# Optimization experiments

Hardware: AMD Instinct MI355X
Metric: run time of the kernel (lower is better)

The kernel has to match this reference:

```python
import jax, jax.numpy as jnp
import numpy as np

N = 50000          # num nodes
E = 800000         # num edges (before self loops)
IN_C = 128
HID = 256          # heads * head_dim
HEADS = 4
HEAD_DIM = HID // HEADS
OUT_C = 64
NEG_SLOPE = 0.2    # PyG GATConv default leaky_relu slope
BN_EPS = 1e-5


def _gat_conv(x, src, dst, W, att_src, att_dst, bias, concat):
    """PyG-style GATConv (with self loops already appended to src/dst).
    x: [N, in_c]; W: [in_c, H*C]; att_src/att_dst: [H, C]; bias: [H*C] or [C]."""
    H, C = att_src.shape
    h = (x @ W).reshape(-1, H, C)                               # [N, H, C]
    a_src = jnp.einsum('nhc,hc->nh', h, att_src)                # [N, H]
    a_dst = jnp.einsum('nhc,hc->nh', h, att_dst)                # [N, H]
    e = jax.nn.leaky_relu(a_src[src] + a_dst[dst], NEG_SLOPE)   # [Et, H]
    # segment softmax over destination nodes (numerically stable)
    m = jax.ops.segment_max(e, dst, num_segments=N)             # [N, H]
    m = jnp.where(jnp.isfinite(m), m, 0.0)
    ex = jnp.exp(e - m[dst])
    denom = jax.ops.segment_sum(ex, dst, num_segments=N)        # [N, H]
    alpha = ex / (denom[dst] + 1e-16)                           # [Et, H]
    msg = alpha[:, :, None] * h[src]                            # [Et, H, C]
    out = jax.ops.segment_sum(msg, dst, num_segments=N)         # [N, H, C]
    out = out.reshape(N, H * C) if concat else out.mean(axis=1)
    return out + bias


def _bn_eval(x, gamma, beta, mean, var):
    return (x - mean) * jax.lax.rsqrt(var + BN_EPS) * gamma + beta


def setup_inputs() -> dict:
    key = jax.random.key(0)
    ks = jax.random.split(key, 16)
    x = jax.random.normal(ks[0], (N, IN_C), dtype=jnp.float32)
    edge_index = jax.random.randint(ks[1], (2, E), 0, N, dtype=jnp.int64)

    def lin(k, fan_in, fan_out):
        s = (1.0 / np.sqrt(fan_in)).astype(np.float32)
        return jax.random.normal(k, (fan_in, fan_out), dtype=jnp.float32) * s

    def att(k, h, c):
        return jax.random.normal(k, (h, c), dtype=jnp.float32) * 0.1

    return {
        'x': x, 'edge_index': edge_index,
        'W0': lin(ks[2], IN_C, HID), 'as0': att(ks[3], HEADS, HEAD_DIM), 'ad0': att(ks[4], HEADS, HEAD_DIM), 'b0': jnp.zeros((HID,), jnp.float32),
        'bn0_g': jnp.ones((HID,), jnp.float32), 'bn0_b': jnp.zeros((HID,), jnp.float32), 'bn0_m': jnp.zeros((HID,), jnp.float32), 'bn0_v': jnp.ones((HID,), jnp.float32),
        'W1': lin(ks[5], HID, HID), 'as1': att(ks[6], HEADS, HEAD_DIM), 'ad1': att(ks[7], HEADS, HEAD_DIM), 'b1': jnp.zeros((HID,), jnp.float32),
        'bn1_g': jnp.ones((HID,), jnp.float32), 'bn1_b': jnp.zeros((HID,), jnp.float32), 'bn1_m': jnp.zeros((HID,), jnp.float32), 'bn1_v': jnp.ones((HID,), jnp.float32),
        'W2': lin(ks[8], HID, OUT_C), 'as2': att(ks[9], 1, OUT_C), 'ad2': att(ks[10], 1, OUT_C), 'b2': jnp.zeros((OUT_C,), jnp.float32),
    }


def reference(x, edge_index, W0, as0, ad0, b0, bn0_g, bn0_b, bn0_m, bn0_v,
              W1, as1, ad1, b1, bn1_g, bn1_b, bn1_m, bn1_v,
              W2, as2, ad2, b2):
    loop = jnp.arange(N, dtype=edge_index.dtype)
    src = jnp.concatenate([edge_index[0], loop])   # PyG add_self_loops=True
    dst = jnp.concatenate([edge_index[1], loop])

    h = _gat_conv(x, src, dst, W0, as0, ad0, b0, concat=True)
    h = jax.nn.elu(_bn_eval(h, bn0_g, bn0_b, bn0_m, bn0_v))   # dropout: eval -> identity
    h = _gat_conv(h, src, dst, W1, as1, ad1, b1, concat=True)
    h = jax.nn.elu(_bn_eval(h, bn1_g, bn1_b, bn1_m, bn1_v))
    out = _gat_conv(h, src, dst, W2, as2, ad2, b2, concat=False)  # heads=1, mean
    return out
```

## Files before the change

### kernel.cpp

```cpp
#include <hip/hip_runtime.h>

#define NN   50000
#define EE   800000
#define ET   850000
#define INC  128
#define HID  256
#define OUTC 64
#define NEG  0.2f
#define BNEPS 1e-5f

typedef __bf16 bf16x8 __attribute__((ext_vector_type(8)));
typedef float  f32x4  __attribute__((ext_vector_type(4)));

static __device__ __forceinline__ float b2f(unsigned short u) {
    return __uint_as_float(((unsigned)u) << 16);
}
static __device__ __forceinline__ unsigned short f2b(float f) {
    unsigned u = __float_as_uint(f);
    unsigned r = u + 0x7FFFu + ((u >> 16) & 1u);
    return (unsigned short)(r >> 16);
}
static __device__ __forceinline__ float leaky(float x) {
    return x > 0.f ? x : NEG * x;
}
static __device__ __forceinline__ float ew(float e) {
    return __expf(fminf(e, 80.f));
}

__global__ void k_init(const int* __restrict__ ei, const unsigned* __restrict__ xw,
                       int* __restrict__ cnt, int* __restrict__ flagW, int* __restrict__ flagB,
                       int nbZ) {
    __shared__ int cs[4];
    int b = blockIdx.x, t = threadIdx.x;
    if (b < nbZ) {
        int i = b * 256 + t;
        if (i < NN) cnt[i] = 0;
    } else if (b == nbZ) {
        int c = 0;
        for (int k = 0; k < 16; k++) {
            int i = t + 256 * k;
            if (ei[2 * i + 1] != 0) c = 1;
        }
        for (int o = 1; o < 64; o <<= 1) c |= __shfl_xor(c, o);
        if ((t & 63) == 0) cs[t >> 6] = c;
        __syncthreads();
        if (t == 0) *flagW = cs[0] | cs[1] | cs[2] | cs[3];
    } else {
        int c = 0;
        for (int i = t; i < 4096; i += 256) {
            unsigned v = (xw[i] >> 8) & 0x7F;
            if (v >= 50 && v <= 67) c++;
        }
        for (int o = 1; o < 64; o <<= 1) c += __shfl_xor(c, o);
        if ((t & 63) == 0) cs[t >> 6] = c;
        __syncthreads();
        if (t == 0) *flagB = (cs[0] + cs[1] + cs[2] + cs[3] > 2048) ? 1 : 0;
    }
}

__global__ void k_params(const void* p0, const void* p1, const void* p2, const void* p3,
                         const void* p4, const void* p5, const void* p6, const void* p7,
                         const void* p8, const void* p9, const void* p10, const void* p11,
                         const void* p12, const void* p13, const void* p14, const void* p15,
                         const void* p16,
                         float* __restrict__ pp, const int* __restrict__ flagB) {
    const void* srcs[17] = {p0,p1,p2,p3,p4,p5,p6,p7,p8,p9,p10,p11,p12,p13,p14,p15,p16};
    int b = blockIdx.x, t = threadIdx.x;
    bool bf = (*flagB != 0);
    if (b < 14) {
        const void* s = srcs[b];
        pp[b * 256 + t] = bf ? b2f(((const unsigned short*)s)[t]) : ((const float*)s)[t];
    } else if (t < 192) {
        int arr = t >> 6, j = t & 63;
        const void* s = srcs[14 + arr];
        pp[14 * 256 + arr * 64 + j] = bf ? b2f(((const unsigned short*)s)[j]) : ((const float*)s)[j];
    }
}

__global__ void k_bulk(const void* __restrict__ W0, const void* __restrict__ W1,
                       const void* __restrict__ W2,
                       unsigned short* __restrict__ WT0, unsigned short* __restrict__ WT1,
                       unsigned short* __restrict__ WT2,
                       const void* __restrict__ x, unsigned short* __restrict__ xb,
                       const int* __restrict__ flagB) {
    int b = blockIdx.x, t = threadIdx.x;
    bool bf = (*flagB != 0);
    if (b < 128) {
        int i = b * 256 + t;
        int k = i >> 8, n = i & 255;
        unsigned short v = bf ? ((const unsigned short*)W0)[i] : f2b(((const float*)W0)[i]);
        WT0[n * INC + k] = v;
    } else if (b < 128 + 256) {
        int i = (b - 128) * 256 + t;
        int k = i >> 8, n = i & 255;
        unsigned short v = bf ? ((const unsigned short*)W1)[i] : f2b(((const float*)W1)[i]);
        WT1[n * HID + k] = v;
    } else if (b < 128 + 256 + 64) {
        int i = (b - 384) * 256 + t;
        int k = i >> 6, n = i & 63;
        unsigned short v = bf ? ((const unsigned short*)W2)[i] : f2b(((const float*)W2)[i]);
        WT2[n * HID + k] = v;
    } else {
        if (bf) return;
        int i = (b - 448) * 256 + t;
        if (i < NN * INC)
            xb[i] = f2b(((const float*)x)[i]);
    }
}

__global__ void k_hist(const int* __restrict__ ei, const int* __restrict__ flagW,
                       int* __restrict__ cnt) {
    int i = blockIdx.x * 256 + threadIdx.x;
    if (i >= ET) return;
    bool w32 = (*flagW != 0);
    int d = (i < EE) ? (w32 ? ei[EE + i] : ei[2 * (EE + i)]) : (i - EE);
    atomicAdd(&cnt[d], 1);
}

static __device__ __forceinline__ int block_scan_incl(int v, int t, int* ws) {
    int lane = t & 63, w = t >> 6;
    int x = v;
    for (int o = 1; o < 64; o <<= 1) {
        int y = __shfl_up(x, o);
        if (lane >= o) x += y;
    }
    if (lane == 63) ws[w] = x;
    __syncthreads();
    if (t == 0) {
        int s = 0;
        for (int k = 0; k < 4; k++) { int tmp = ws[k]; ws[k] = s; s += tmp; }
    }
    __syncthreads();
    return x + ws[w];
}

__global__ void k_scan_a(const int* __restrict__ cnt, int* __restrict__ rowptr, int* __restrict__ bsum) {
    __shared__ int ws[4];
    int t = threadIdx.x, b = blockIdx.x;
    int i = b * 256 + t;
    int v = (i < NN) ? cnt[i] : 0;
    int incl = block_scan_incl(v, t, ws);
    if (i < NN) rowptr[i] = incl - v;
    if (t == 255) bsum[b] = incl;
}

__global__ void k_scan_b(int* __restrict__ bsum, int nb) {
    __shared__ int ws[4];
    int t = threadIdx.x;
    int v = (t < nb) ? bsum[t] : 0;
    int incl = block_scan_incl(v, t, ws);
    if (t < nb) bsum[t] = incl - v;
}

__global__ void k_scan_c(int* __restrict__ rowptr, const int* __restrict__ bsum, int* __restrict__ cursor) {
    int t = threadIdx.x, b = blockIdx.x;
    int i = b * 256 + t;
    if (i < NN) {
        int r = rowptr[i] + bsum[b];
        rowptr[i] = r;
        cursor[i] = r;
    }
    if (i == 0) rowptr[NN] = ET;
}

__global__ void k_scatter(const int* __restrict__ ei, const int* __restrict__ flagW,
                          int* __restrict__ cursor, int* __restrict__ esrc) {
    int i = blockIdx.x * 256 + threadIdx.x;
    if (i >= ET) return;
    bool w32 = (*flagW != 0);
    int s, d;
    if (i < EE) {
        if (w32) { s = ei[i];     d = ei[EE + i]; }
        else     { s = ei[2 * i]; d = ei[2 * (EE + i)]; }
    } else {
        s = d = i - EE;
    }
    int p = atomicAdd(&cursor[d], 1);
    esrc[p] = s;
}

template<int NC, int NH>
__global__ __launch_bounds__(256) void k_gemm(const unsigned short* __restrict__ Amain,
                                              const void* __restrict__ Aalt,
                                              const int* __restrict__ flagB,
                                              const unsigned short* __restrict__ WT,
                                              unsigned short* __restrict__ H,
                                              float* __restrict__ asrc, float* __restrict__ adst,
                                              const float* __restrict__ asv, const float* __restrict__ adv,
                                              int M, int K) {
    __shared__ __align__(16) unsigned short As[128 * 40];
    __shared__ __align__(16) unsigned short Bs[64 * 40];
    const unsigned short* A = (*flagB) ? (const unsigned short*)Aalt : Amain;
    int t = threadIdx.x;
    int bm = blockIdx.x, bn = blockIdx.y;
    int lane = t & 63, wave = t >> 6;
    int m16 = lane & 15, quad = lane >> 4;

    f32x4 acc[2][4];
    for (int a = 0; a < 2; a++) for (int b = 0; b < 4; b++) acc[a][b] = (f32x4){0.f, 0.f, 0.f, 0.f};

    int arow = t >> 1, ahalf = t & 1;
    int brow = t >> 2, bq = t & 3;
    long gArow = (long)bm * 128 + arow;

    for (int k0 = 0; k0 < K; k0 += 32) {
        uint4 av0 = {0u, 0u, 0u, 0u}, av1 = {0u, 0u, 0u, 0u};
        if (gArow < M) {
            const unsigned short* ap = A + gArow * (size_t)K + k0 + ahalf * 16;
            av0 = *(const uint4*)(ap);
            av1 = *(const uint4*)(ap + 8);
        }
        uint4 bv = *(const uint4*)(WT + ((size_t)bn * 64 + brow) * K + k0 + bq * 8);
        *(uint4*)&As[arow * 40 + ahalf * 16]     = av0;
        *(uint4*)&As[arow * 40 + ahalf * 16 + 8] = av1;
        *(uint4*)&Bs[brow * 40 + bq * 8]         = bv;
        __syncthreads();
        int wrow = wave * 32;
        bf16x8 af[2], bf[4];
        for (int mt = 0; mt < 2; mt++)
            af[mt] = *(const bf16x8*)&As[(wrow + mt * 16 + m16) * 40 + quad * 8];
        for (int nt = 0; nt < 4; nt++)
            bf[nt] = *(const bf16x8*)&Bs[(nt * 16 + m16) * 40 + quad * 8];
        for (int mt = 0; mt < 2; mt++)
            for (int nt = 0; nt < 4; nt++)
                acc[mt][nt] = __builtin_amdgcn_mfma_f32_16x16x32_bf16(af[mt], bf[nt], acc[mt][nt], 0, 0, 0);
        __syncthreads();
    }

    float asc[4], adc[4];
    for (int nt = 0; nt < 4; nt++) {
        int col = bn * 64 + nt * 16 + m16;
        asc[nt] = asv[col];
        adc[nt] = adv[col];
    }
    for (int mt = 0; mt < 2; mt++) {
        int gR0 = bm * 128 + wave * 32 + mt * 16 + quad * 4;
        for (int r = 0; r < 4; r++) {
            int gR = gR0 + r;
            float ps = 0.f, pd = 0.f;
            for (int nt = 0; nt < 4; nt++) {
                float v = acc[mt][nt][r];
                ps += v * asc[nt];
                pd += v * adc[nt];
            }
            for (int o = 1; o < 16; o <<= 1) { ps += __shfl_xor(ps, o); pd += __shfl_xor(pd, o); }
            if (m16 == 0 && gR < M) {
                asrc[(size_t)gR * NH + bn] = ps;
                adst[(size_t)gR * NH + bn] = pd;
            }
            if (gR < M) {
                for (int nt = 0; nt < 4; nt++) {
                    int gC = bn * 64 + nt * 16 + m16;
                    H[(size_t)gR * NC + gC] = f2b(acc[mt][nt][r]);
                }
            }
        }
    }
}

__global__ void k_agg4(const unsigned short* __restrict__ h,
                       const float* __restrict__ asrc, const float* __restrict__ adst,
                       const int* __restrict__ rowptr, const int* __restrict__ esrc,
                       const float* __restrict__ bias,
                       const float* __restrict__ bng, const float* __restrict__ bnb,
                       const float* __restrict__ bnm, const float* __restrict__ bnv,
                       unsigned short* __restrict__ act) {
    int t = threadIdx.x;
    int wave = t >> 6, lane = t & 63;
    int node = blockIdx.x * 4 + wave;
    if (node >= NN) return;
    int e0 = rowptr[node], deg = rowptr[node + 1] - e0;
    int hd = lane >> 4, li = lane & 15;
    int wsel = lane & 48;
    float adh = adst[(size_t)node * 4 + hd];
    const size_t lc = (size_t)lane * 4;

    float den = 0.f, a0 = 0.f, a1 = 0.f, a2 = 0.f, a3 = 0.f;

    for (int c = 0; c < deg; c += 16) {
        int n = min(16, deg - c);
        float w = 0.f; int s = 0;
        if (li < n) {
            s = esrc[e0 + c + li];
            float e = asrc[(size_t)s * 4 + hd];
            w = ew(leaky(e + adh));
        }
        float wsum = w;
        wsum += __shfl_xor(wsum, 1);
        wsum += __shfl_xor(wsum, 2);
        wsum += __shfl_xor(wsum, 4);
        wsum += __shfl_xor(wsum, 8);
        den += wsum;
        int j = 0;
        for (; j + 8 <= n; j += 8) {
            int s0 = __shfl(s, j),     s1 = __shfl(s, j + 1);
            int s2 = __shfl(s, j + 2), s3 = __shfl(s, j + 3);
            int s4 = __shfl(s, j + 4), s5 = __shfl(s, j + 5);
            int s6 = __shfl(s, j + 6), s7 = __shfl(s, j + 7);
            float w0 = __shfl(w, wsel + j),     w1 = __shfl(w, wsel + j + 1);
            float w2 = __shfl(w, wsel + j + 2), w3 = __shfl(w, wsel + j + 3);
            float w4 = __shfl(w, wsel + j + 4), w5 = __shfl(w, wsel + j + 5);
            float w6 = __shfl(w, wsel + j + 6), w7 = __shfl(w, wsel + j + 7);
            ushort4 h0 = *(const ushort4*)(h + (size_t)s0 * HID + lc);
            ushort4 h1 = *(const ushort4*)(h + (size_t)s1 * HID + lc);
            ushort4 h2 = *(const ushort4*)(h + (size_t)s2 * HID + lc);
            ushort4 h3 = *(const ushort4*)(h + (size_t)s3 * HID + lc);
            ushort4 h4 = *(const ushort4*)(h + (size_t)s4 * HID + lc);
            ushort4 h5 = *(const ushort4*)(h + (size_t)s5 * HID + lc);
            ushort4 h6 = *(const ushort4*)(h + (size_t)s6 * HID + lc);
            ushort4 h7 = *(const ushort4*)(h + (size_t)s7 * HID + lc);
            a0 += w0 * b2f(h0.x) + w1 * b2f(h1.x) + w2 * b2f(h2.x) + w3 * b2f(h3.x)
                + w4 * b2f(h4.x) + w5 * b2f(h5.x) + w6 * b2f(h6.x) + w7 * b2f(h7.x);
            a1 += w0 * b2f(h0.y) + w1 * b2f(h1.y) + w2 * b2f(h2.y) + w3 * b2f(h3.y)
                + w4 * b2f(h4.y) + w5 * b2f(h5.y) + w6 * b2f(h6.y) + w7 * b2f(h7.y);
            a2 += w0 * b2f(h0.z) + w1 * b2f(h1.z) + w2 * b2f(h2.z) + w3 * b2f(h3.z)
                + w4 * b2f(h4.z) + w5 * b2f(h5.z) + w6 * b2f(h6.z) + w7 * b2f(h7.z);
            a3 += w0 * b2f(h0.w) + w1 * b2f(h1.w) + w2 * b2f(h2.w) + w3 * b2f(h3.w)
                + w4 * b2f(h4.w) + w5 * b2f(h5.w) + w6 * b2f(h6.w) + w7 * b2f(h7.w);
        }
        for (; j + 4 <= n; j += 4) {
            int s0 = __shfl(s, j),     s1 = __shfl(s, j + 1);
            int s2 = __shfl(s, j + 2), s3 = __shfl(s, j + 3);
            float w0 = __shfl(w, wsel + j),     w1 = __shfl(w, wsel + j + 1);
            float w2 = __shfl(w, wsel + j + 2), w3 = __shfl(w, wsel + j + 3);
            ushort4 h0 = *(const ushort4*)(h + (size_t)s0 * HID + lc);
            ushort4 h1 = *(const ushort4*)(h + (size_t)s1 * HID + lc);
            ushort4 h2 = *(const ushort4*)(h + (size_t)s2 * HID + lc);
            ushort4 h3 = *(const ushort4*)(h + (size_t)s3 * HID + lc);
            a0 += w0 * b2f(h0.x) + w1 * b2f(h1.x) + w2 * b2f(h2.x) + w3 * b2f(h3.x);
            a1 += w0 * b2f(h0.y) + w1 * b2f(h1.y) + w2 * b2f(h2.y) + w3 * b2f(h3.y);
            a2 += w0 * b2f(h0.z) + w1 * b2f(h1.z) + w2 * b2f(h2.z) + w3 * b2f(h3.z);
            a3 += w0 * b2f(h0.w) + w1 * b2f(h1.w) + w2 * b2f(h2.w) + w3 * b2f(h3.w);
        }
        for (; j < n; j++) {
            int sj = __shfl(s, j);
            float wj = __shfl(w, wsel + j);
            ushort4 hv = *(const ushort4*)(h + (size_t)sj * HID + lc);
            a0 += wj * b2f(hv.x); a1 += wj * b2f(hv.y);
            a2 += wj * b2f(hv.z); a3 += wj * b2f(hv.w);
        }
    }
    float inv = 1.f / (den + 1e-16f);
    int c0 = lane * 4;
    float o[4] = {a0 * inv, a1 * inv, a2 * inv, a3 * inv};
    unsigned short res[4];
    for (int j = 0; j < 4; j++) {
        int c = c0 + j;
        float val = o[j] + bias[c];
        val = (val - bnm[c]) * rsqrtf(bnv[c] + BNEPS) * bng[c] + bnb[c];
        val = val > 0.f ? val : expm1f(val);
        res[j] = f2b(val);
    }
    *(ushort4*)(act + (size_t)node * HID + c0) = *(ushort4*)res;
}

__global__ void k_agg1(const unsigned short* __restrict__ h,
                       const float* __restrict__ asrc, const float* __restrict__ adst,
                       const int* __restrict__ rowptr, const int* __restrict__ esrc,
                       const float* __restrict__ bias,
                       void* __restrict__ outp, const int* __restrict__ flagB) {
    int t = threadIdx.x;
    int wave = t >> 6, lane = t & 63;
    int node = blockIdx.x * 4 + wave;
    if (node >= NN) return;
    int e0 = rowptr[node], deg = rowptr[node + 1] - e0;
    float ad = adst[node];

    float den = 0.f, acc = 0.f;
    for (int c = 0; c < deg; c += 64) {
        int n = min(64, deg - c);
        float w = 0.f; int s = 0;
        if (lane < n) {
            s = esrc[e0 + c + lane];
            w = ew(leaky(asrc[s] + ad));
        }
        float wsum = w;
        for (int o = 1; o < 64; o <<= 1) wsum += __shfl_xor(wsum, o);
        den += wsum;
        int j = 0;
        for (; j + 8 <= n; j += 8) {
            int s0 = __shfl(s, j),     s1 = __shfl(s, j + 1);
            int s2 = __shfl(s, j + 2), s3 = __shfl(s, j + 3);
            int s4 = __shfl(s, j + 4), s5 = __shfl(s, j + 5);
            int s6 = __shfl(s, j + 6), s7 = __shfl(s, j + 7);
            float w0 = __shfl(w, j),     w1 = __shfl(w, j + 1);
            float w2 = __shfl(w, j + 2), w3 = __shfl(w, j + 3);
            float w4 = __shfl(w, j + 4), w5 = __shfl(w, j + 5);
            float w6 = __shfl(w, j + 6), w7 = __shfl(w, j + 7);
            float h0 = b2f(h[(size_t)s0 * OUTC + lane]);
            float h1 = b2f(h[(size_t)s1 * OUTC + lane]);
            float h2 = b2f(h[(size_t)s2 * OUTC + lane]);
            float h3 = b2f(h[(size_t)s3 * OUTC + lane]);
            float h4 = b2f(h[(size_t)s4 * OUTC + lane]);
            float h5 = b2f(h[(size_t)s5 * OUTC + lane]);
            float h6 = b2f(h[(size_t)s6 * OUTC + lane]);
            float h7 = b2f(h[(size_t)s7 * OUTC + lane]);
            acc += w0 * h0 + w1 * h1 + w2 * h2 + w3 * h3
                 + w4 * h4 + w5 * h5 + w6 * h6 + w7 * h7;
        }
        for (; j < n; j++) {
            int sj = __shfl(s, j);
            float wj = __shfl(w, j);
            acc += wj * b2f(h[(size_t)sj * OUTC + lane]);
        }
    }
    float val = acc / (den + 1e-16f) + bias[lane];
    if (*flagB) ((unsigned short*)outp)[(size_t)node * OUTC + lane] = f2b(val);
    else        ((float*)outp)[(size_t)node * OUTC + lane] = val;
}

extern "C" void kernel_launch(void* const* d_in, const int* in_sizes, int n_in,
                              void* d_out, int out_size, void* d_ws, size_t ws_size,
                              hipStream_t stream) {
    const void* x  = d_in[0];
    const int*  ei = (const int*)d_in[1];
    const void* W0 = d_in[2];
    const void* W1 = d_in[10];
    const void* W2 = d_in[18];

    char* ws = (char*)d_ws;
    size_t off = 0;
    auto alloc = [&](size_t n) { void* p = ws + off; off += (n + 255) & ~(size_t)255; return p; };

    unsigned short* xb  = (unsigned short*)alloc((size_t)NN * INC * 2);
    unsigned short* h   = (unsigned short*)alloc((size_t)NN * HID * 2);
    unsigned short* act = (unsigned short*)alloc((size_t)NN * HID * 2);
    unsigned short* WT0 = (unsigned short*)alloc((size_t)HID * INC * 2);
    unsigned short* WT1 = (unsigned short*)alloc((size_t)HID * HID * 2);
    unsigned short* WT2 = (unsigned short*)alloc((size_t)OUTC * HID * 2);
    float*          pp  = (float*)alloc((size_t)(14 * 256 + 3 * 64) * 4);
    float*  asrc   = (float*)alloc((size_t)NN * 4 * 4);
    float*  adst   = (float*)alloc((size_t)NN * 4 * 4);
    int*    cnt    = (int*)alloc((size_t)(NN + 2) * 4);
    int*    rowptr = (int*)alloc((size_t)(NN + 1) * 4);
    int*    cursor = (int*)alloc((size_t)NN * 4);
    int*    esrc   = (int*)alloc((size_t)ET * 4);
    int*    bsum   = (int*)alloc(256 * 4);
    int*    flagW  = cnt + NN;
    int*    flagB  = cnt + NN + 1;

    float* P0 = pp;
    float* P1 = pp + 7 * 256;
    float* P2 = pp + 14 * 256;

    const int nbN = (NN + 255) / 256;
    const int nbE = (ET + 255) / 256;
    const int nbA = (NN + 3) / 4;
    const int nbBulk = 448 + (NN * INC + 255) / 256;
    dim3 gemmGrid0((NN + 127) / 128, HID / 64);
    dim3 gemmGrid2((NN + 127) / 128, 1);

    k_init<<<nbN + 2, 256, 0, stream>>>(ei, (const unsigned*)x, cnt, flagW, flagB, nbN);
    k_hist<<<nbE, 256, 0, stream>>>(ei, flagW, cnt);
    k_scan_a<<<nbN, 256, 0, stream>>>(cnt, rowptr, bsum);
    k_scan_b<<<1, 256, 0, stream>>>(bsum, nbN);
    k_scan_c<<<nbN, 256, 0, stream>>>(rowptr, bsum, cursor);
    k_scatter<<<nbE, 256, 0, stream>>>(ei, flagW, cursor, esrc);

    k_params<<<15, 256, 0, stream>>>(d_in[3], d_in[4], d_in[5], d_in[6], d_in[7], d_in[8], d_in[9],
                                     d_in[11], d_in[12], d_in[13], d_in[14], d_in[15], d_in[16], d_in[17],
                                     d_in[19], d_in[20], d_in[21], pp, flagB);
    k_bulk<<<nbBulk, 256, 0, stream>>>(W0, W1, W2, WT0, WT1, WT2, x, xb, flagB);

    k_gemm<HID, 4><<<gemmGrid0, 256, 0, stream>>>(xb, x, flagB, WT0, h, asrc, adst,
                                                  P0 + 0, P0 + 256, NN, INC);
    k_agg4<<<nbA, 256, 0, stream>>>(h, asrc, adst, rowptr, esrc,
                                    P0 + 512, P0 + 768, P0 + 1024, P0 + 1280, P0 + 1536, act);

    k_gemm<HID, 4><<<gemmGrid0, 256, 0, stream>>>(act, act, flagB, WT1, h, asrc, adst,
                                                  P1 + 0, P1 + 256, NN, HID);
    k_agg4<<<nbA, 256, 0, stream>>>(h, asrc, adst, rowptr, esrc,
                                    P1 + 512, P1 + 768, P1 + 1024, P1 + 1280, P1 + 1536, act);

    k_gemm<OUTC, 1><<<gemmGrid2, 256, 0, stream>>>(act, act, flagB, WT2, h, asrc, adst,
                                                   P2 + 0, P2 + 64, NN, HID);
    k_agg1<<<nbA, 256, 0, stream>>>(h, asrc, adst, rowptr, esrc, P2 + 128, d_out, flagB);
}
```

Before: 507.4 us.

## Merge param/weight prep kernels and prefetch next edge chunk in aggregation

Fuses the parameter-conversion and weight-transpose kernels into a single prep launch, replacing the runtime-indexed pointer array with a switch. In the aggregation kernels, the next chunk's source indices and attention logits are loaded before the current chunk is processed, so their latency overlaps the gather work. The 8-wide unrolled gather loops are dropped in favour of the 4-wide loops, which lowers register pressure but leaves fewer loads in flight per iteration.

```diff
diff --git a/kernel.cpp b/kernel.cpp
--- a/kernel.cpp
+++ b/kernel.cpp
@@ -58,51 +58,61 @@
     }
 }
 
-__global__ void k_params(const void* p0, const void* p1, const void* p2, const void* p3,
-                         const void* p4, const void* p5, const void* p6, const void* p7,
-                         const void* p8, const void* p9, const void* p10, const void* p11,
-                         const void* p12, const void* p13, const void* p14, const void* p15,
-                         const void* p16,
-                         float* __restrict__ pp, const int* __restrict__ flagB) {
-    const void* srcs[17] = {p0,p1,p2,p3,p4,p5,p6,p7,p8,p9,p10,p11,p12,p13,p14,p15,p16};
-    int b = blockIdx.x, t = threadIdx.x;
-    bool bf = (*flagB != 0);
-    if (b < 14) {
-        const void* s = srcs[b];
-        pp[b * 256 + t] = bf ? b2f(((const unsigned short*)s)[t]) : ((const float*)s)[t];
-    } else if (t < 192) {
-        int arr = t >> 6, j = t & 63;
-        const void* s = srcs[14 + arr];
-        pp[14 * 256 + arr * 64 + j] = bf ? b2f(((const unsigned short*)s)[j]) : ((const float*)s)[j];
-    }
-}
-
-__global__ void k_bulk(const void* __restrict__ W0, const void* __restrict__ W1,
-                       const void* __restrict__ W2,
+__global__ void k_prep(const void* as0, const void* ad0, const void* b0, const void* g0,
+                       const void* be0, const void* m0, const void* v0,
+                       const void* as1, const void* ad1, const void* b1, const void* g1,
+                       const void* be1, const void* m1, const void* v1,
+                       const void* as2, const void* ad2, const void* b2,
+                       const void* W0, const void* W1, const void* W2,
                        unsigned short* __restrict__ WT0, unsigned short* __restrict__ WT1,
                        unsigned short* __restrict__ WT2,
                        const void* __restrict__ x, unsigned short* __restrict__ xb,
-                       const int* __restrict__ flagB) {
+                       float* __restrict__ pp, const int* __restrict__ flagB) {
     int b = blockIdx.x, t = threadIdx.x;
     bool bf = (*flagB != 0);
-    if (b < 128) {
-        int i = b * 256 + t;
+    auto cv = [&](const void* s, int i) -> float {
+        return bf ? b2f(((const unsigned short*)s)[i]) : ((const float*)s)[i];
+    };
+    if (b < 14) {
+        float v;
+        switch (b) {
+            case 0:  v = cv(as0, t); break;
+            case 1:  v = cv(ad0, t); break;
+            case 2:  v = cv(b0, t);  break;
+            case 3:  v = cv(g0, t);  break;
+            case 4:  v = cv(be0, t); break;
+            case 5:  v = cv(m0, t);  break;
+            case 6:  v = cv(v0, t);  break;
+            case 7:  v = cv(as1, t); break;
+            case 8:  v = cv(ad1, t); break;
+            case 9:  v = cv(b1, t);  break;
+            case 10: v = cv(g1, t);  break;
+            case 11: v = cv(be1, t); break;
+            case 12: v = cv(m1, t);  break;
+            default: v = cv(v1, t);  break;
+        }
+        pp[b * 256 + t] = v;
+    } else if (b == 14) {
+        if (t < 192) {
+            int arr = t >> 6, j = t & 63;
+            float v = (arr == 0) ? cv(as2, j) : (arr == 1) ? cv(ad2, j) : cv(b2, j);
+            pp[14 * 256 + arr * 64 + j] = v;
+        }
+    } else if (b < 15 + 128) {
+        int i = (b - 15) * 256 + t;
         int k = i >> 8, n = i & 255;
-        unsigned short v = bf ? ((const unsigned short*)W0)[i] : f2b(((const float*)W0)[i]);
-        WT0[n * INC + k] = v;
-    } else if (b < 128 + 256) {
-        int i = (b - 128) * 256 + t;
+        WT0[n * INC + k] = bf ? ((const unsigned short*)W0)[i] : f2b(((const float*)W0)[i]);
+    } else if (b < 15 + 128 + 256) {
+        int i = (b - 143) * 256 + t;
         int k = i >> 8, n = i & 255;
-        unsigned short v = bf ? ((const unsigned short*)W1)[i] : f2b(((const float*)W1)[i]);
-        WT1[n * HID + k] = v;
-    } else if (b < 128 + 256 + 64) {
-        int i = (b - 384) * 256 + t;
+        WT1[n * HID + k] = bf ? ((const unsigned short*)W1)[i] : f2b(((const float*)W1)[i]);
+    } else if (b < 15 + 128 + 256 + 64) {
+        int i = (b - 399) * 256 + t;
         int k = i >> 6, n = i & 63;
-        unsigned short v = bf ? ((const unsigned short*)W2)[i] : f2b(((const float*)W2)[i]);
-        WT2[n * HID + k] = v;
+        WT2[n * HID + k] = bf ? ((const unsigned short*)W2)[i] : f2b(((const float*)W2)[i]);
     } else {
         if (bf) return;
-        int i = (b - 448) * 256 + t;
+        int i = (b - 463) * 256 + t;
         if (i < NN * INC)
             xb[i] = f2b(((const float*)x)[i]);
     }
@@ -277,13 +287,20 @@
 
     float den = 0.f, a0 = 0.f, a1 = 0.f, a2 = 0.f, a3 = 0.f;
 
+    int n = min(16, deg);
+    int s = 0; float e = 0.f;
+    if (li < n) {
+        s = esrc[e0 + li];
+        e = asrc[(size_t)s * 4 + hd];
+    }
+
     for (int c = 0; c < deg; c += 16) {
-        int n = min(16, deg - c);
-        float w = 0.f; int s = 0;
-        if (li < n) {
-            s = esrc[e0 + c + li];
-            float e = asrc[(size_t)s * 4 + hd];
-            w = ew(leaky(e + adh));
+        float w = (li < n) ? ew(leaky(e + adh)) : 0.f;
+        int n2 = min(16, deg - (c + 16));
+        int sN = 0; float eN = 0.f;
+        if (li < n2) {
+            sN = esrc[e0 + c + 16 + li];
+            eN = asrc[(size_t)sN * 4 + hd];
         }
         float wsum = w;
         wsum += __shfl_xor(wsum, 1);
@@ -292,32 +309,6 @@
         wsum += __shfl_xor(wsum, 8);
         den += wsum;
         int j = 0;
-        for (; j + 8 <= n; j += 8) {
-            int s0 = __shfl(s, j),     s1 = __shfl(s, j + 1);
-            int s2 = __shfl(s, j + 2), s3 = __shfl(s, j + 3);
-            int s4 = __shfl(s, j + 4), s5 = __shfl(s, j + 5);
-            int s6 = __shfl(s, j + 6), s7 = __shfl(s, j + 7);
-            float w0 = __shfl(w, wsel + j),     w1 = __shfl(w, wsel + j + 1);
-            float w2 = __shfl(w, wsel + j + 2), w3 = __shfl(w, wsel + j + 3);
-            float w4 = __shfl(w, wsel + j + 4), w5 = __shfl(w, wsel + j + 5);
-            float w6 = __shfl(w, wsel + j + 6), w7 = __shfl(w, wsel + j + 7);
-            ushort4 h0 = *(const ushort4*)(h + (size_t)s0 * HID + lc);
-            ushort4 h1 = *(const ushort4*)(h + (size_t)s1 * HID + lc);
-            ushort4 h2 = *(const ushort4*)(h + (size_t)s2 * HID + lc);
-            ushort4 h3 = *(const ushort4*)(h + (size_t)s3 * HID + lc);
-            ushort4 h4 = *(const ushort4*)(h + (size_t)s4 * HID + lc);
-            ushort4 h5 = *(const ushort4*)(h + (size_t)s5 * HID + lc);
-            ushort4 h6 = *(const ushort4*)(h + (size_t)s6 * HID + lc);
-            ushort4 h7 = *(const ushort4*)(h + (size_t)s7 * HID + lc);
-            a0 += w0 * b2f(h0.x) + w1 * b2f(h1.x) + w2 * b2f(h2.x) + w3 * b2f(h3.x)
-                + w4 * b2f(h4.x) + w5 * b2f(h5.x) + w6 * b2f(h6.x) + w7 * b2f(h7.x);
-            a1 += w0 * b2f(h0.y) + w1 * b2f(h1.y) + w2 * b2f(h2.y) + w3 * b2f(h3.y)
-                + w4 * b2f(h4.y) + w5 * b2f(h5.y) + w6 * b2f(h6.y) + w7 * b2f(h7.y);
-            a2 += w0 * b2f(h0.z) + w1 * b2f(h1.z) + w2 * b2f(h2.z) + w3 * b2f(h3.z)
-                + w4 * b2f(h4.z) + w5 * b2f(h5.z) + w6 * b2f(h6.z) + w7 * b2f(h7.z);
-            a3 += w0 * b2f(h0.w) + w1 * b2f(h1.w) + w2 * b2f(h2.w) + w3 * b2f(h3.w)
-                + w4 * b2f(h4.w) + w5 * b2f(h5.w) + w6 * b2f(h6.w) + w7 * b2f(h7.w);
-        }
         for (; j + 4 <= n; j += 4) {
             int s0 = __shfl(s, j),     s1 = __shfl(s, j + 1);
             int s2 = __shfl(s, j + 2), s3 = __shfl(s, j + 3);
@@ -339,6 +330,7 @@
             a0 += wj * b2f(hv.x); a1 += wj * b2f(hv.y);
             a2 += wj * b2f(hv.z); a3 += wj * b2f(hv.w);
         }
+        s = sN; e = eN; n = n2;
     }
     float inv = 1.f / (den + 1e-16f);
     int c0 = lane * 4;
@@ -367,42 +359,43 @@
     float ad = adst[node];
 
     float den = 0.f, acc = 0.f;
+
+    int n = min(64, deg);
+    int s = 0; float e = 0.f;
+    if (lane < n) {
+        s = esrc[e0 + lane];
+        e = asrc[s];
+    }
+
     for (int c = 0; c < deg; c += 64) {
-        int n = min(64, deg - c);
-        float w = 0.f; int s = 0;
-        if (lane < n) {
-            s = esrc[e0 + c + lane];
-            w = ew(leaky(asrc[s] + ad));
+        float w = (lane < n) ? ew(leaky(e + ad)) : 0.f;
+        int n2 = min(64, deg - (c + 64));
+        int sN = 0; float eN = 0.f;
+        if (lane < n2) {
+            sN = esrc[e0 + c + 64 + lane];
+            eN = asrc[sN];
         }
         float wsum = w;
         for (int o = 1; o < 64; o <<= 1) wsum += __shfl_xor(wsum, o);
         den += wsum;
         int j = 0;
-        for (; j + 8 <= n; j += 8) {
+        for (; j + 4 <= n; j += 4) {
             int s0 = __shfl(s, j),     s1 = __shfl(s, j + 1);
             int s2 = __shfl(s, j + 2), s3 = __shfl(s, j + 3);
-            int s4 = __shfl(s, j + 4), s5 = __shfl(s, j + 5);
-            int s6 = __shfl(s, j + 6), s7 = __shfl(s, j + 7);
             float w0 = __shfl(w, j),     w1 = __shfl(w, j + 1);
             float w2 = __shfl(w, j + 2), w3 = __shfl(w, j + 3);
-            float w4 = __shfl(w, j + 4), w5 = __shfl(w, j + 5);
-            float w6 = __shfl(w, j + 6), w7 = __shfl(w, j + 7);
             float h0 = b2f(h[(size_t)s0 * OUTC + lane]);
             float h1 = b2f(h[(size_t)s1 * OUTC + lane]);
             float h2 = b2f(h[(size_t)s2 * OUTC + lane]);
             float h3 = b2f(h[(size_t)s3 * OUTC + lane]);
-            float h4 = b2f(h[(size_t)s4 * OUTC + lane]);
-            float h5 = b2f(h[(size_t)s5 * OUTC + lane]);
-            float h6 = b2f(h[(size_t)s6 * OUTC + lane]);
-            float h7 = b2f(h[(size_t)s7 * OUTC + lane]);
-            acc += w0 * h0 + w1 * h1 + w2 * h2 + w3 * h3
-                 + w4 * h4 + w5 * h5 + w6 * h6 + w7 * h7;
+            acc += w0 * h0 + w1 * h1 + w2 * h2 + w3 * h3;
         }
         for (; j < n; j++) {
             int sj = __shfl(s, j);
             float wj = __shfl(w, j);
             acc += wj * b2f(h[(size_t)sj * OUTC + lane]);
         }
+        s = sN; e = eN; n = n2;
     }
     float val = acc / (den + 1e-16f) + bias[lane];
     if (*flagB) ((unsigned short*)outp)[(size_t)node * OUTC + lane] = f2b(val);
@@ -446,7 +439,7 @@
     const int nbN = (NN + 255) / 256;
     const int nbE = (ET + 255) / 256;
     const int nbA = (NN + 3) / 4;
-    const int nbBulk = 448 + (NN * INC + 255) / 256;
+    const int nbPrep = 463 + (NN * INC + 255) / 256;
     dim3 gemmGrid0((NN + 127) / 128, HID / 64);
     dim3 gemmGrid2((NN + 127) / 128, 1);
 
@@ -457,10 +450,10 @@
     k_scan_c<<<nbN, 256, 0, stream>>>(rowptr, bsum, cursor);
     k_scatter<<<nbE, 256, 0, stream>>>(ei, flagW, cursor, esrc);
 
-    k_params<<<15, 256, 0, stream>>>(d_in[3], d_in[4], d_in[5], d_in[6], d_in[7], d_in[8], d_in[9],
-                                     d_in[11], d_in[12], d_in[13], d_in[14], d_in[15], d_in[16], d_in[17],
-                                     d_in[19], d_in[20], d_in[21], pp, flagB);
-    k_bulk<<<nbBulk, 256, 0, stream>>>(W0, W1, W2, WT0, WT1, WT2, x, xb, flagB);
+    k_prep<<<nbPrep, 256, 0, stream>>>(d_in[3], d_in[4], d_in[5], d_in[6], d_in[7], d_in[8], d_in[9],
+                                       d_in[11], d_in[12], d_in[13], d_in[14], d_in[15], d_in[16], d_in[17],
+                                       d_in[19], d_in[20], d_in[21],
+                                       W0, W1, W2, WT0, WT1, WT2, x, xb, pp, flagB);
 
     k_gemm<HID, 4><<<gemmGrid0, 256, 0, stream>>>(xb, x, flagB, WT0, h, asrc, adst,
                                                   P0 + 0, P0 + 256, NN, INC);
```

New measurement: 488.8 us. 1.04x faster.
